# Kernel tuning notes

Measured on AMD Instinct MI355X. Metric: run time of the kernel, lower is better.

Reference implementation:

```python
import jax, jax.numpy as jnp
import numpy as np

B, L, HID = 2, 2048, 2560
H, HKV, DH = 32, 8, 128
G = H // HKV  # GQA groups = 4
EPS = 1e-6
THETA = 1000000.0


def setup_inputs() -> dict:
    key = jax.random.key(0)
    ks = jax.random.split(key, 6)
    x = jax.random.normal(ks[0], (B, L, HID), dtype=jnp.float32)
    Wq = jax.random.normal(ks[1], (HID, H * DH), dtype=jnp.float32) * 0.02
    Wk = jax.random.normal(ks[2], (HID, HKV * DH), dtype=jnp.float32) * 0.02
    Wv = jax.random.normal(ks[3], (HID, HKV * DH), dtype=jnp.float32) * 0.02
    Wo = jax.random.normal(ks[4], (H * DH, HID), dtype=jnp.float32) * 0.02
    q_norm_w = jnp.ones((DH,), dtype=jnp.float32)
    k_norm_w = jnp.ones((DH,), dtype=jnp.float32)
    # RoPE tables, theta=1e6, non-interleaved (half-split) layout
    inv_freq = 1.0 / (THETA ** (jnp.arange(0, DH, 2, dtype=jnp.float32) / DH))
    pos = jnp.arange(L, dtype=jnp.float32)
    freqs = pos[:, None] * inv_freq[None, :]              # [L, DH/2]
    emb = jnp.concatenate([freqs, freqs], axis=-1)        # [L, DH]
    cos = jnp.broadcast_to(jnp.cos(emb)[None], (B, L, DH))
    sin = jnp.broadcast_to(jnp.sin(emb)[None], (B, L, DH))
    return {"x": x, "Wq": Wq, "Wk": Wk, "Wv": Wv, "Wo": Wo,
            "q_norm_w": q_norm_w, "k_norm_w": k_norm_w,
            "cos": cos, "sin": sin}


def _rmsnorm(x, w):
    xf = x.astype(jnp.float32)
    var = jnp.mean(xf * xf, axis=-1, keepdims=True)
    return (xf * jax.lax.rsqrt(var + EPS)).astype(x.dtype) * w


def _rotate_half(x):
    x1, x2 = jnp.split(x, 2, axis=-1)
    return jnp.concatenate([-x2, x1], axis=-1)


def reference(x, Wq, Wk, Wv, Wo, q_norm_w, k_norm_w, cos, sin):
    b, l, _ = x.shape
    q = (x @ Wq).reshape(b, l, H, DH)
    k = (x @ Wk).reshape(b, l, HKV, DH)
    v = (x @ Wv).reshape(b, l, HKV, DH).transpose(0, 2, 1, 3)   # [B,HKV,L,DH]
    q = _rmsnorm(q, q_norm_w).transpose(0, 2, 1, 3)             # [B,H,L,DH]
    k = _rmsnorm(k, k_norm_w).transpose(0, 2, 1, 3)             # [B,HKV,L,DH]
    c = cos[:, None]  # [B,1,L,DH]
    s = sin[:, None]
    q = q * c + _rotate_half(q) * s
    k = k * c + _rotate_half(k) * s
    # GQA SDPA, causal
    qg = q.reshape(b, HKV, G, l, DH)
    scale = 1.0 / np.sqrt(DH)
    scores = jnp.einsum('bkgqd,bkmd->bkgqm', qg, k) * scale     # [B,HKV,G,L,L]
    causal = jnp.tril(jnp.ones((l, l), dtype=bool))
    scores = jnp.where(causal, scores, jnp.finfo(scores.dtype).min)
    attn = jax.nn.softmax(scores, axis=-1)
    out = jnp.einsum('bkgqm,bkmd->bkgqd', attn, v)              # [B,HKV,G,L,DH]
    out = out.reshape(b, H, l, DH).transpose(0, 2, 1, 3).reshape(b, l, H * DH)
    return out @ Wo
```

## Files before the change

### kernel.cpp

```cpp
#include <hip/hip_runtime.h>

typedef unsigned short u16;
typedef unsigned int u32;
using bf16x8 = __attribute__((ext_vector_type(8))) __bf16;
using f32x4  = __attribute__((ext_vector_type(4))) float;

typedef const void __attribute__((address_space(1)))* gas1p;
typedef void __attribute__((address_space(3)))* las3p;

__device__ __forceinline__ void gload16(const void* g, void* l) {
  __builtin_amdgcn_global_load_lds((gas1p)g, (las3p)l, 16, 0, 0);
}

__device__ __forceinline__ u16 f2bf(float f) {
  union { float f; unsigned u; } v; v.f = f;
  unsigned r = v.u + 0x7FFFu + ((v.u >> 16) & 1u);
  return (u16)(r >> 16);
}
__device__ __forceinline__ float bf2f(u16 h) {
  union { unsigned u; float f; } v; v.u = ((unsigned)h) << 16;
  return v.f;
}

__global__ __launch_bounds__(256)
void cvt_f32_bf16(const float4* __restrict__ in, uint2* __restrict__ out, int n4) {
  int i = blockIdx.x * 256 + threadIdx.x;
  if (i >= n4) return;
  float4 v = in[i];
  uint2 o;
  o.x = (unsigned)f2bf(v.x) | ((unsigned)f2bf(v.y) << 16);
  o.y = (unsigned)f2bf(v.z) | ((unsigned)f2bf(v.w) << 16);
  out[i] = o;
}

__global__ __launch_bounds__(256)
void transpose_w(const float* __restrict__ in, u16* __restrict__ out, int R, int C) {
  __shared__ float tile[32][33];
  const int tx = threadIdx.x & 31, ty = threadIdx.x >> 5;
  const int r0 = blockIdx.y * 32, c0 = blockIdx.x * 32;
#pragma unroll
  for (int i = 0; i < 4; i++)
    tile[ty + i * 8][tx] = in[(size_t)(r0 + ty + i * 8) * C + c0 + tx];
  __syncthreads();
#pragma unroll
  for (int i = 0; i < 4; i++)
    out[(size_t)(c0 + ty + i * 8) * R + r0 + tx] = f2bf(tile[tx][ty + i * 8]);
}

__global__ __launch_bounds__(256)
void transpose_v(const u16* __restrict__ QKV, u16* __restrict__ Vt) {
  __shared__ u16 tile[32][34];
  const int tx = threadIdx.x & 31, ty = threadIdx.x >> 5;
  const int l0 = blockIdx.x * 32, d0 = blockIdx.y * 32;
  const int bkv = blockIdx.z;
  const int b = bkv >> 3, kvh = bkv & 7;
#pragma unroll
  for (int i = 0; i < 4; i++)
    tile[ty + i * 8][tx] =
        QKV[(size_t)(b * 2048 + l0 + ty + i * 8) * 6144 + 5120 + kvh * 128 + d0 + tx];
  __syncthreads();
#pragma unroll
  for (int i = 0; i < 4; i++)
    Vt[((size_t)bkv * 128 + d0 + ty + i * 8) * 2048 + l0 + tx] = tile[tx][ty + i * 8];
}

__global__ __launch_bounds__(256)
void norm_rope(const u16* __restrict__ QKV, const float* __restrict__ qw,
               const float* __restrict__ kw, const float* __restrict__ cosp,
               const float* __restrict__ sinp, u16* __restrict__ Qr,
               u16* __restrict__ Kr) {
  const int rid = blockIdx.x * 4 + (threadIdx.x >> 6);
  const int lane = threadIdx.x & 63;
  const int head = rid % 40;
  const int bl = rid / 40;
  const int b = bl >> 11, l = bl & 2047;
  const u16* src; const float* w; u16* dst; float scale;
  if (head < 32) {
    src = QKV + (size_t)bl * 6144 + head * 128;
    w = qw;
    dst = Qr + ((size_t)(b * 32 + head) * 2048 + l) * 128;
    scale = 0.08838834764831845f;
  } else {
    const int kvh = head - 32;
    src = QKV + (size_t)bl * 6144 + 4096 + kvh * 128;
    w = kw;
    dst = Kr + ((size_t)(b * 8 + kvh) * 2048 + l) * 128;
    scale = 1.0f;
  }
  float lo = bf2f(src[lane]);
  float hi = bf2f(src[lane + 64]);
  float ss = lo * lo + hi * hi;
#pragma unroll
  for (int m = 1; m < 64; m <<= 1) ss += __shfl_xor(ss, m, 64);
  const float rstd = rsqrtf(ss * (1.0f / 128.0f) + 1e-6f) * scale;
  const float nlo = lo * rstd * w[lane];
  const float nhi = hi * rstd * w[lane + 64];
  const float* cb = cosp + (size_t)bl * 128;
  const float* sb = sinp + (size_t)bl * 128;
  dst[lane]      = f2bf(nlo * cb[lane]      - nhi * sb[lane]);
  dst[lane + 64] = f2bf(nhi * cb[lane + 64] + nlo * sb[lane + 64]);
}

#define SMEMA(c) (smem + (c) * 16384)
#define SMEMB(c) (smem + 32768 + (c) * (NJ * 8192))
#define STGA(c, kk)                                                         \
  { gload16(Ab + stgo + (kk), SMEMA(c) + (tid << 4));                       \
    gload16(Ab + stgo + (size_t)64 * K + (kk), SMEMA(c) + 8192 + (tid << 4)); }
#define STGB(c, kk, q)                                                      \
  gload16(Bb + stgo + (size_t)(q) * 64 * K + (kk),                          \
          SMEMB(c) + ((q) << 13) + (tid << 4))
#define LDA(c)                                                              \
  { _Pragma("unroll") for (int i = 0; i < 4; i++)                           \
    _Pragma("unroll") for (int ks = 0; ks < 2; ks++) {                      \
      const int row = wm * 64 + i * 16 + fr;                                \
      af[i][ks] = *(const bf16x8*)(SMEMA(c) + row * 128 +                   \
                                   ((((ks << 2) + fq) ^ (row & 7)) << 4)); } }
#define LDB(c, j, d)                                                        \
  { _Pragma("unroll") for (int ks = 0; ks < 2; ks++) {                      \
      const int row = (j) * 64 + wn * 16 + fr;                              \
      d[ks] = *(const bf16x8*)(SMEMB(c) + row * 128 +                       \
                               ((((ks << 2) + fq) ^ (row & 7)) << 4)); } }
#define MMAJ(j, bv)                                                         \
  _Pragma("unroll") for (int i = 0; i < 4; i++) {                           \
    acc[i][j] = __builtin_amdgcn_mfma_f32_16x16x32_bf16(af[i][0], bv[0],    \
                                                        acc[i][j], 0, 0, 0);\
    acc[i][j] = __builtin_amdgcn_mfma_f32_16x16x32_bf16(af[i][1], bv[1],    \
                                                        acc[i][j], 0, 0, 0); }
#define BAR __builtin_amdgcn_s_barrier()
#define WLG { asm volatile("s_waitcnt lgkmcnt(0)" ::: "memory");            \
              __builtin_amdgcn_sched_barrier(0); }
#define WVMn(n) asm volatile("s_waitcnt vmcnt(" #n ")" ::: "memory")
#define SP1 __builtin_amdgcn_s_setprio(1)
#define SP0 __builtin_amdgcn_s_setprio(0)

template <int NJ, typename CT>
__global__ __launch_bounds__(512, 2)
void gemmN(const u16* __restrict__ A, const u16* __restrict__ Bt,
           CT* __restrict__ C, int N, int K, int MT) {
  extern __shared__ char smem[];
  const int tid = threadIdx.x, lane = tid & 63, wid = tid >> 6;
  const int wm = wid >> 2, wn = wid & 3;
  const int fr = lane & 15, fq = lane >> 4;
  const int qx = (int)gridDim.x >> 3;
  const int wg = ((int)blockIdx.x & 7) * qx + ((int)blockIdx.x >> 3);
  const int bx = wg / MT, by = wg - bx * MT;
  const int m0 = by * 128, n0 = bx * (NJ * 64);
  const u16* Ab = A + (size_t)m0 * K;
  const u16* Bb = Bt + (size_t)n0 * K;
  const size_t stgo =
      (size_t)(tid >> 3) * K + (size_t)(((tid & 7) ^ ((tid >> 3) & 7)) << 3);

  f32x4 acc[4][NJ];
#pragma unroll
  for (int i = 0; i < 4; i++)
#pragma unroll
    for (int j = 0; j < NJ; j++)
#pragma unroll
      for (int r = 0; r < 4; r++) acc[i][j][r] = 0.f;

  bf16x8 af[4][2], b0[2], b1[2];
  const int NT = K >> 6;

  STGA(0, 0);
#pragma unroll
  for (int q2 = 0; q2 < NJ; q2++) STGB(0, 0, q2);
  if constexpr (NJ == 6) { WVMn(4); } else { WVMn(3); }
  BAR;

  for (int t = 0; t < NT; t++) {
    const int c = t & 1, cn = c ^ 1;
    const int kn = ((t + 1 == NT) ? 0 : (t + 1)) << 6;
    LDA(c); LDB(c, 0, b0); LDB(c, 1, b1);
    STGA(cn, kn); STGB(cn, kn, 0);
    if constexpr (NJ == 6) { WVMn(5); } else { WVMn(4); }
    BAR; WLG; SP1; MMAJ(0, b0); MMAJ(1, b1); SP0; BAR;
    LDB(c, 2, b0); LDB(c, 3, b1);
    STGB(cn, kn, 1); STGB(cn, kn, 2);
    if constexpr (NJ == 6) { STGB(cn, kn, 3); WVMn(6); } else { WVMn(5); }
    BAR; WLG; SP1; MMAJ(2, b0); MMAJ(3, b1); SP0; BAR;
    LDB(c, 4, b0);
    if constexpr (NJ == 6) {
      LDB(c, 5, b1);
      STGB(cn, kn, 4); STGB(cn, kn, 5); WVMn(4);
    } else {
      STGB(cn, kn, 3); STGB(cn, kn, 4); WVMn(3);
    }
    BAR; WLG; SP1; MMAJ(4, b0);
    if constexpr (NJ == 6) MMAJ(5, b1);
    SP0; BAR;
  }
  WVMn(0);

#pragma unroll
  for (int i = 0; i < 4; i++) {
    const int row0 = m0 + wm * 64 + i * 16 + fq * 4;
#pragma unroll
    for (int j = 0; j < NJ; j++) {
      const int col = n0 + j * 64 + wn * 16 + fr;
#pragma unroll
      for (int r = 0; r < 4; r++) {
        const size_t idx = (size_t)(row0 + r) * N + col;
        if constexpr (sizeof(CT) == 2) C[idx] = f2bf(acc[i][j][r]);
        else C[idx] = acc[i][j][r];
      }
    }
  }
}

__global__ __launch_bounds__(256, 2)
void attn_fwd(const u16* __restrict__ Qr, const u16* __restrict__ Kr,
              const u16* __restrict__ Vt, u16* __restrict__ AO) {
  const int L = 2048, DH = 128;
  __shared__ u16 Ks[2][64 * 128];
  __shared__ u16 Vs[2][128 * 64];
  const int tid = threadIdx.x, lane = tid & 63, wid = tid >> 6;
  const int fr = lane & 15, fq = lane >> 4;
  const int j = blockIdx.x >> 4;
  const int grp = blockIdx.x & 15;
  const int kvh = grp >> 1, b = grp & 1;
  const int h = kvh * 4 + wid;

  const u16* Kbase = Kr + (size_t)(b * 8 + kvh) * L * DH;
  const u16* Vbase = Vt + (size_t)(b * 8 + kvh) * DH * L;

  int Dly[4], kOff[4], vOff[4];
#pragma unroll
  for (int p = 0; p < 4; p++) {
    const int D = (tid + p * 256) * 16;
    Dly[p] = D;
    const int kr = D >> 8, kc = ((D >> 4) & 15) ^ (kr & 7);
    kOff[p] = kr * 128 + kc * 8;
    const int vr = D >> 7, vc = ((D >> 4) & 7) ^ (vr & 7);
    vOff[p] = vr * 2048 + vc * 8;
  }

  const bool B5 = (lane & 32) != 0;
  const bool A4 = (lane & 16) != 0;

  auto stage = [&](int kt, int bufi) {
    const int k0 = kt * 64;
#pragma unroll
    for (int p = 0; p < 4; p++) {
      gload16(Kbase + (size_t)k0 * 128 + kOff[p], (char*)&Ks[bufi][0] + Dly[p]);
      gload16(Vbase + k0 + vOff[p], (char*)&Vs[bufi][0] + Dly[p]);
    }
  };

  for (int half = 0; half < 2; half++) {
    const int t = half ? 63 - j : j;
    const int nk = (t >> 1) + 1;

    bf16x8 qf[2][4];
#pragma unroll
    for (int g = 0; g < 2; g++) {
      const int qq = t * 32 + g * 16 + fr;
      const u16* qbase = Qr + ((size_t)(b * 32 + h) * L + qq) * DH + fq * 8;
#pragma unroll
      for (int dt = 0; dt < 4; dt++) qf[g][dt] = *(const bf16x8*)(qbase + dt * 32);
    }
    asm volatile("s_waitcnt vmcnt(0)" ::: "memory");

    f32x4 o[2][8];
#pragma unroll
    for (int g = 0; g < 2; g++)
#pragma unroll
      for (int d = 0; d < 8; d++)
#pragma unroll
        for (int r = 0; r < 4; r++) o[g][d][r] = 0.f;
    float mrow[2] = {-__builtin_huge_valf(), -__builtin_huge_valf()};
    float lrow[2] = {0.f, 0.f};

    __builtin_amdgcn_s_barrier();
    stage(0, 0);
    int cur = 0;

    for (int kt = 0; kt < nk; kt++) {
      if (kt + 1 < nk) {
        stage(kt + 1, cur ^ 1);
        asm volatile("s_waitcnt vmcnt(8)" ::: "memory");
      } else {
        asm volatile("s_waitcnt vmcnt(0)" ::: "memory");
      }
      __builtin_amdgcn_s_barrier();

      const u16* KsB = &Ks[cur][0];
      const u16* VsB = &Vs[cur][0];
      const int k0 = kt * 64;

      f32x4 s4[2][4];
#pragma unroll
      for (int g = 0; g < 2; g++)
#pragma unroll
        for (int ni = 0; ni < 4; ni++)
#pragma unroll
          for (int r = 0; r < 4; r++) s4[g][ni][r] = 0.f;
#pragma unroll
      for (int ni = 0; ni < 4; ni++) {
        const int krow = ni * 16 + fr;
        const int sw = (krow & 7) << 4;
#pragma unroll
        for (int dt = 0; dt < 4; dt++) {
          const int off = (krow * 256 + dt * 64 + fq * 16) ^ sw;
          bf16x8 kf = *(const bf16x8*)((const char*)KsB + off);
          s4[0][ni] = __builtin_amdgcn_mfma_f32_16x16x32_bf16(kf, qf[0][dt], s4[0][ni], 0, 0, 0);
          s4[1][ni] = __builtin_amdgcn_mfma_f32_16x16x32_bf16(kf, qf[1][dt], s4[1][ni], 0, 0, 0);
        }
      }

      if (kt == nk - 1) {
#pragma unroll
        for (int g = 0; g < 2; g++) {
          const int qq = t * 32 + g * 16 + fr;
#pragma unroll
          for (int ni = 0; ni < 4; ni++)
#pragma unroll
            for (int r = 0; r < 4; r++)
              if (k0 + ni * 16 + fq * 4 + r > qq) s4[g][ni][r] = -1e30f;
        }
      }

      bf16x8 pb[2][2];
#pragma unroll
      for (int g = 0; g < 2; g++) {
        float mt = s4[g][0][0];
#pragma unroll
        for (int ni = 0; ni < 4; ni++)
#pragma unroll
          for (int r = 0; r < 4; r++) mt = fmaxf(mt, s4[g][ni][r]);
        mt = fmaxf(mt, __shfl_xor(mt, 16, 64));
        mt = fmaxf(mt, __shfl_xor(mt, 32, 64));

        if (!__all(mt <= mrow[g] + 8.f)) {
          const float mn = fmaxf(mrow[g], mt);
          const float corr = exp2f((mrow[g] - mn) * 1.44269504f);
          mrow[g] = mn;
          lrow[g] *= corr;
#pragma unroll
          for (int d = 0; d < 8; d++)
#pragma unroll
            for (int r = 0; r < 4; r++) o[g][d][r] *= corr;
        }

        const float ml = mrow[g] * 1.44269504f;
        float rs = 0.f;
#pragma unroll
        for (int ni = 0; ni < 4; ni++)
#pragma unroll
          for (int r = 0; r < 4; r++) {
            const float pv = exp2f(fmaf(s4[g][ni][r], 1.44269504f, -ml));
            s4[g][ni][r] = pv;
            rs += pv;
          }
        rs += __shfl_xor(rs, 16, 64);
        rs += __shfl_xor(rs, 32, 64);
        lrow[g] += rs;

        u32 pk[4][2];
#pragma unroll
        for (int ni = 0; ni < 4; ni++) {
          pk[ni][0] = __builtin_amdgcn_perm(__float_as_uint(s4[g][ni][1]),
                                            __float_as_uint(s4[g][ni][0]), 0x07060302u);
          pk[ni][1] = __builtin_amdgcn_perm(__float_as_uint(s4[g][ni][3]),
                                            __float_as_uint(s4[g][ni][2]), 0x07060302u);
        }
#pragma unroll
        for (int ks = 0; ks < 2; ks++) {
          u32 r00 = pk[2 * ks + 0][0], r01 = pk[2 * ks + 0][1];
          u32 r10 = pk[2 * ks + 1][0], r11 = pk[2 * ks + 1][1];
          u32 e0 = __shfl_xor(B5 ? r00 : r10, 32, 64);
          u32 t00 = B5 ? e0 : r00, t10 = B5 ? r10 : e0;
          u32 e1 = __shfl_xor(B5 ? r01 : r11, 32, 64);
          u32 t01 = B5 ? e1 : r01, t11 = B5 ? r11 : e1;
          u32 e2 = __shfl_xor(A4 ? t00 : t10, 16, 64);
          u32 u00 = A4 ? e2 : t00, u10 = A4 ? t10 : e2;
          u32 e3 = __shfl_xor(A4 ? t01 : t11, 16, 64);
          u32 u01 = A4 ? e3 : t01, u11 = A4 ? t11 : e3;
          union { u32 u[4]; bf16x8 v; } pbv;
          pbv.u[0] = u00; pbv.u[1] = u01; pbv.u[2] = u10; pbv.u[3] = u11;
          pb[g][ks] = pbv.v;
        }
      }

#pragma unroll
      for (int d = 0; d < 8; d++) {
        const int vrow = d * 16 + fr;
        const int sw = (vrow & 7) << 4;
#pragma unroll
        for (int ks = 0; ks < 2; ks++) {
          const int off = (vrow * 128 + ks * 64 + fq * 16) ^ sw;
          bf16x8 vf = *(const bf16x8*)((const char*)VsB + off);
          o[0][d] = __builtin_amdgcn_mfma_f32_16x16x32_bf16(vf, pb[0][ks], o[0][d], 0, 0, 0);
          o[1][d] = __builtin_amdgcn_mfma_f32_16x16x32_bf16(vf, pb[1][ks], o[1][d], 0, 0, 0);
        }
      }
      __builtin_amdgcn_s_barrier();
      cur ^= 1;
    }

#pragma unroll
    for (int g = 0; g < 2; g++) {
      const float inv = 1.f / lrow[g];
      const int qq = t * 32 + g * 16 + fr;
      u16* obase = AO + ((size_t)b * L + qq) * 4096 + h * 128 + fq * 4;
#pragma unroll
      for (int d = 0; d < 8; d++) {
        uint2 w;
        w.x = (u32)f2bf(o[g][d][0] * inv) | ((u32)f2bf(o[g][d][1] * inv) << 16);
        w.y = (u32)f2bf(o[g][d][2] * inv) | ((u32)f2bf(o[g][d][3] * inv) << 16);
        *(uint2*)(obase + d * 16) = w;
      }
    }
  }
}

extern "C" void kernel_launch(void* const* d_in, const int* in_sizes, int n_in,
                              void* d_out, int out_size, void* d_ws, size_t ws_size,
                              hipStream_t stream) {
  const float* x    = (const float*)d_in[0];
  const float* Wq   = (const float*)d_in[1];
  const float* Wk   = (const float*)d_in[2];
  const float* Wv   = (const float*)d_in[3];
  const float* Wo   = (const float*)d_in[4];
  const float* qw   = (const float*)d_in[5];
  const float* kw   = (const float*)d_in[6];
  const float* cosp = (const float*)d_in[7];
  const float* sinp = (const float*)d_in[8];
  float* out = (float*)d_out;
  char* ws = (char*)d_ws;

  u16* xb    = (u16*)(ws);
  u16* WqkvT = (u16*)(ws + 20971520);
  u16* WoT   = (u16*)(ws + 52428800);
  u16* QKV   = (u16*)(ws + 73400320);
  u16* AO    = QKV;
  u16* Qrr   = (u16*)(ws + 123731968);
  u16* Krr   = (u16*)(ws + 157286400);
  u16* Vtt   = (u16*)(ws + 165675008);

  hipFuncSetAttribute(reinterpret_cast<const void*>(&gemmN<6, u16>),
                      hipFuncAttributeMaxDynamicSharedMemorySize, 131072);
  hipFuncSetAttribute(reinterpret_cast<const void*>(&gemmN<5, float>),
                      hipFuncAttributeMaxDynamicSharedMemorySize, 114688);

  cvt_f32_bf16<<<10240, 256, 0, stream>>>((const float4*)x, (uint2*)xb, 2621440);
  transpose_w<<<dim3(128, 80), 256, 0, stream>>>(Wq, WqkvT, 2560, 4096);
  transpose_w<<<dim3(32, 80), 256, 0, stream>>>(Wk, WqkvT + (size_t)4096 * 2560, 2560, 1024);
  transpose_w<<<dim3(32, 80), 256, 0, stream>>>(Wv, WqkvT + (size_t)5120 * 2560, 2560, 1024);
  transpose_w<<<dim3(80, 128), 256, 0, stream>>>(Wo, WoT, 4096, 2560);

  gemmN<6, u16><<<512, 512, 131072, stream>>>(xb, WqkvT, QKV, 6144, 2560, 32);

  norm_rope<<<40960, 256, 0, stream>>>(QKV, qw, kw, cosp, sinp, Qrr, Krr);
  transpose_v<<<dim3(64, 4, 16), 256, 0, stream>>>(QKV, Vtt);

  attn_fwd<<<dim3(512), 256, 0, stream>>>(Qrr, Krr, Vtt, AO);

  gemmN<5, float><<<256, 512, 114688, stream>>>(AO, WoT, out, 2560, 4096, 32);
}
```

Baseline: 423.6 us.

## Replace K64 GEMM with K32-step GEMM using smaller tiles and higher occupancy

Swaps the two projection GEMMs to a new kernel that steps K by 32 instead of 64, uses a 2x4 wave layout with templated MI/NJ tile sizes, and drops LDS from 128KB to 48KB or 36KB. Launch bounds rise to 4 blocks per CU, and grids grow (768 and 512 blocks), so more tiles run at once and the wave count is better balanced. The cost is smaller tiles with less data reuse per byte loaded, twice as many barrier/sync steps per K, and an unswizzled LDS layout that may cause bank conflicts.

```diff
diff --git a/kernel.cpp b/kernel.cpp
--- a/kernel.cpp
+++ b/kernel.cpp
@@ -101,31 +101,6 @@
   dst[lane + 64] = f2bf(nhi * cb[lane + 64] + nlo * sb[lane + 64]);
 }
 
-#define SMEMA(c) (smem + (c) * 16384)
-#define SMEMB(c) (smem + 32768 + (c) * (NJ * 8192))
-#define STGA(c, kk)                                                         \
-  { gload16(Ab + stgo + (kk), SMEMA(c) + (tid << 4));                       \
-    gload16(Ab + stgo + (size_t)64 * K + (kk), SMEMA(c) + 8192 + (tid << 4)); }
-#define STGB(c, kk, q)                                                      \
-  gload16(Bb + stgo + (size_t)(q) * 64 * K + (kk),                          \
-          SMEMB(c) + ((q) << 13) + (tid << 4))
-#define LDA(c)                                                              \
-  { _Pragma("unroll") for (int i = 0; i < 4; i++)                           \
-    _Pragma("unroll") for (int ks = 0; ks < 2; ks++) {                      \
-      const int row = wm * 64 + i * 16 + fr;                                \
-      af[i][ks] = *(const bf16x8*)(SMEMA(c) + row * 128 +                   \
-                                   ((((ks << 2) + fq) ^ (row & 7)) << 4)); } }
-#define LDB(c, j, d)                                                        \
-  { _Pragma("unroll") for (int ks = 0; ks < 2; ks++) {                      \
-      const int row = (j) * 64 + wn * 16 + fr;                              \
-      d[ks] = *(const bf16x8*)(SMEMB(c) + row * 128 +                       \
-                               ((((ks << 2) + fq) ^ (row & 7)) << 4)); } }
-#define MMAJ(j, bv)                                                         \
-  _Pragma("unroll") for (int i = 0; i < 4; i++) {                           \
-    acc[i][j] = __builtin_amdgcn_mfma_f32_16x16x32_bf16(af[i][0], bv[0],    \
-                                                        acc[i][j], 0, 0, 0);\
-    acc[i][j] = __builtin_amdgcn_mfma_f32_16x16x32_bf16(af[i][1], bv[1],    \
-                                                        acc[i][j], 0, 0, 0); }
 #define BAR __builtin_amdgcn_s_barrier()
 #define WLG { asm volatile("s_waitcnt lgkmcnt(0)" ::: "memory");            \
               __builtin_amdgcn_sched_barrier(0); }
@@ -133,70 +108,111 @@
 #define SP1 __builtin_amdgcn_s_setprio(1)
 #define SP0 __builtin_amdgcn_s_setprio(0)
 
-template <int NJ, typename CT>
-__global__ __launch_bounds__(512, 2)
-void gemmN(const u16* __restrict__ A, const u16* __restrict__ Bt,
-           CT* __restrict__ C, int N, int K, int MT) {
+template <int MI, int NJ, typename CT>
+__global__ __launch_bounds__(512, 4)
+void gemmK32(const u16* __restrict__ A, const u16* __restrict__ Bt,
+             CT* __restrict__ C, int N, int K, int MT) {
   extern __shared__ char smem[];
+  constexpr int ASZ = MI * 4096;
+  constexpr int BSZ = NJ * 2048;
+  constexpr int J1 = (MI == 4) ? 2 : 3;
   const int tid = threadIdx.x, lane = tid & 63, wid = tid >> 6;
-  const int wm = wid >> 2, wn = wid & 3;
+  const int wm = wid >> 1, wn = wid & 1;
   const int fr = lane & 15, fq = lane >> 4;
   const int qx = (int)gridDim.x >> 3;
   const int wg = ((int)blockIdx.x & 7) * qx + ((int)blockIdx.x >> 3);
   const int bx = wg / MT, by = wg - bx * MT;
-  const int m0 = by * 128, n0 = bx * (NJ * 64);
+  const int m0 = by * (MI * 64), n0 = bx * (NJ * 32);
   const u16* Ab = A + (size_t)m0 * K;
   const u16* Bb = Bt + (size_t)n0 * K;
-  const size_t stgo =
-      (size_t)(tid >> 3) * K + (size_t)(((tid & 7) ^ ((tid >> 3) & 7)) << 3);
-
-  f32x4 acc[4][NJ];
-#pragma unroll
-  for (int i = 0; i < 4; i++)
+
+  char* const A0 = smem;
+  char* const B0 = smem + 2 * ASZ;
+#define ABUF(c) (A0 + (c) * ASZ)
+#define BBUF(c) (B0 + (c) * BSZ)
+
+  const int sF = (tid >> 2) * K + (tid & 3) * 8;
+  const int tq = tid & 255;
+  const int sH = (tq >> 2) * K + (tq & 3) * 8;
+  const int to = tid & 127;
+  const int sO = (to >> 2) * K + (to & 3) * 8;
+
+  const int aRd = (wm * MI * 16 + fr) * 64 + fq * 16;
+  const int bRd = (wn * 16 + fr) * 64 + fq * 16;
+
+  f32x4 acc[MI][NJ];
+#pragma unroll
+  for (int i = 0; i < MI; i++)
 #pragma unroll
     for (int j = 0; j < NJ; j++)
 #pragma unroll
       for (int r = 0; r < 4; r++) acc[i][j][r] = 0.f;
 
-  bf16x8 af[4][2], b0[2], b1[2];
-  const int NT = K >> 6;
-
-  STGA(0, 0);
-#pragma unroll
-  for (int q2 = 0; q2 < NJ; q2++) STGB(0, 0, q2);
-  if constexpr (NJ == 6) { WVMn(4); } else { WVMn(3); }
+  bf16x8 af[MI], bfr[3];
+  const int NT = K >> 5;
+
+  auto stageP1 = [&](int c2, int kk) {
+    if constexpr (MI == 4) {
+      gload16(Ab + sF + kk, ABUF(c2) + (tid << 4));
+      gload16(Ab + sF + (size_t)128 * K + kk, ABUF(c2) + 8192 + (tid << 4));
+    } else {
+      gload16(Ab + sF + kk, ABUF(c2) + (tid << 4));
+      gload16(Bb + sF + kk, BBUF(c2) + (tid << 4));
+    }
+  };
+  auto stageP2 = [&](int c2, int kk) {
+    if constexpr (MI == 4) {
+      gload16(Bb + sH + kk, BBUF(c2) + (tq << 4));
+      gload16(Bb + sH + (size_t)64 * K + kk, BBUF(c2) + 4096 + (tq << 4));
+    } else {
+      gload16(Bb + sO + (size_t)128 * K + kk, BBUF(c2) + 8192 + (to << 4));
+    }
+  };
+
+  stageP1(0, 0);
+  stageP2(0, 0);
+  WVMn(1);
   BAR;
 
   for (int t = 0; t < NT; t++) {
     const int c = t & 1, cn = c ^ 1;
-    const int kn = ((t + 1 == NT) ? 0 : (t + 1)) << 6;
-    LDA(c); LDB(c, 0, b0); LDB(c, 1, b1);
-    STGA(cn, kn); STGB(cn, kn, 0);
-    if constexpr (NJ == 6) { WVMn(5); } else { WVMn(4); }
-    BAR; WLG; SP1; MMAJ(0, b0); MMAJ(1, b1); SP0; BAR;
-    LDB(c, 2, b0); LDB(c, 3, b1);
-    STGB(cn, kn, 1); STGB(cn, kn, 2);
-    if constexpr (NJ == 6) { STGB(cn, kn, 3); WVMn(6); } else { WVMn(5); }
-    BAR; WLG; SP1; MMAJ(2, b0); MMAJ(3, b1); SP0; BAR;
-    LDB(c, 4, b0);
-    if constexpr (NJ == 6) {
-      LDB(c, 5, b1);
-      STGB(cn, kn, 4); STGB(cn, kn, 5); WVMn(4);
-    } else {
-      STGB(cn, kn, 3); STGB(cn, kn, 4); WVMn(3);
-    }
-    BAR; WLG; SP1; MMAJ(4, b0);
-    if constexpr (NJ == 6) MMAJ(5, b1);
+    const int kn = ((t + 1 == NT) ? 0 : (t + 1)) << 5;
+#pragma unroll
+    for (int i = 0; i < MI; i++)
+      af[i] = *(const bf16x8*)(ABUF(c) + aRd + i * 1024);
+#pragma unroll
+    for (int j = 0; j < J1; j++)
+      bfr[j] = *(const bf16x8*)(BBUF(c) + bRd + j * 2048);
+    stageP1(cn, kn);
+    WVMn(2);
+    BAR; WLG; SP1;
+#pragma unroll
+    for (int j = 0; j < J1; j++)
+#pragma unroll
+      for (int i = 0; i < MI; i++)
+        acc[i][j] = __builtin_amdgcn_mfma_f32_16x16x32_bf16(af[i], bfr[j], acc[i][j], 0, 0, 0);
+    SP0; BAR;
+#pragma unroll
+    for (int j = J1; j < NJ; j++)
+      bfr[j - J1] = *(const bf16x8*)(BBUF(c) + bRd + j * 2048);
+    stageP2(cn, kn);
+    WVMn(1);
+    BAR; WLG; SP1;
+#pragma unroll
+    for (int j = J1; j < NJ; j++)
+#pragma unroll
+      for (int i = 0; i < MI; i++)
+        acc[i][j] = __builtin_amdgcn_mfma_f32_16x16x32_bf16(af[i], bfr[j - J1], acc[i][j], 0, 0, 0);
     SP0; BAR;
   }
   WVMn(0);
 
 #pragma unroll
-  for (int i = 0; i < 4; i++) {
-    const int row0 = m0 + wm * 64 + i * 16 + fq * 4;
+  for (int i = 0; i < MI; i++) {
+    const int row0 = m0 + (wm * MI + i) * 16 + fq * 4;
 #pragma unroll
     for (int j = 0; j < NJ; j++) {
-      const int col = n0 + j * 64 + wn * 16 + fr;
+      const int col = n0 + (j * 2 + wn) * 16 + fr;
 #pragma unroll
       for (int r = 0; r < 4; r++) {
         const size_t idx = (size_t)(row0 + r) * N + col;
@@ -205,6 +221,8 @@
       }
     }
   }
+#undef ABUF
+#undef BBUF
 }
 
 __global__ __launch_bounds__(256, 2)
@@ -437,10 +455,10 @@
   u16* Krr   = (u16*)(ws + 157286400);
   u16* Vtt   = (u16*)(ws + 165675008);
 
-  hipFuncSetAttribute(reinterpret_cast<const void*>(&gemmN<6, u16>),
-                      hipFuncAttributeMaxDynamicSharedMemorySize, 131072);
-  hipFuncSetAttribute(reinterpret_cast<const void*>(&gemmN<5, float>),
-                      hipFuncAttributeMaxDynamicSharedMemorySize, 114688);
+  hipFuncSetAttribute(reinterpret_cast<const void*>(&gemmK32<4, 4, u16>),
+                      hipFuncAttributeMaxDynamicSharedMemorySize, 49152);
+  hipFuncSetAttribute(reinterpret_cast<const void*>(&gemmK32<2, 5, float>),
+                      hipFuncAttributeMaxDynamicSharedMemorySize, 36864);
 
   cvt_f32_bf16<<<10240, 256, 0, stream>>>((const float4*)x, (uint2*)xb, 2621440);
   transpose_w<<<dim3(128, 80), 256, 0, stream>>>(Wq, WqkvT, 2560, 4096);
@@ -448,12 +466,12 @@
   transpose_w<<<dim3(32, 80), 256, 0, stream>>>(Wv, WqkvT + (size_t)5120 * 2560, 2560, 1024);
   transpose_w<<<dim3(80, 128), 256, 0, stream>>>(Wo, WoT, 4096, 2560);
 
-  gemmN<6, u16><<<512, 512, 131072, stream>>>(xb, WqkvT, QKV, 6144, 2560, 32);
+  gemmK32<4, 4, u16><<<768, 512, 49152, stream>>>(xb, WqkvT, QKV, 6144, 2560, 16);
 
   norm_rope<<<40960, 256, 0, stream>>>(QKV, qw, kw, cosp, sinp, Qrr, Krr);
   transpose_v<<<dim3(64, 4, 16), 256, 0, stream>>>(QKV, Vtt);
 
   attn_fwd<<<dim3(512), 256, 0, stream>>>(Qrr, Krr, Vtt, AO);
 
-  gemmN<5, float><<<256, 512, 114688, stream>>>(AO, WoT, out, 2560, 4096, 32);
-}
+  gemmK32<2, 5, float><<<512, 512, 36864, stream>>>(AO, WoT, out, 2560, 4096, 32);
+}
```

After: 470.1 us. +11.0%, slower.
